# Kernel optimization log

Hardware: AMD Instinct MI355X
Metric: run time of the kernel (lower is better)

## Reference

```python
import jax, jax.numpy as jnp
import numpy as np

B, NVIS, NHID, NCLASS = 2048, 2048, 1024, 64


def setup_inputs() -> dict:
    key = jax.random.key(0)
    k1, k2, k3, k4, k5 = jax.random.split(key, 5)
    return {
        "v": jax.random.normal(k1, (B, NVIS), dtype=jnp.float32),
        "W": jax.random.normal(k2, (NVIS, NHID), dtype=jnp.float32),
        "c": jax.random.normal(k3, (1, NHID), dtype=jnp.float32),
        "d": jax.random.normal(k4, (1, NCLASS), dtype=jnp.float32),
        "U": jax.random.normal(k5, (NCLASS, NHID), dtype=jnp.float32),
    }


def reference(v, W, c, d, U):
    # precomputed_factor: [B, nhid]
    pre = jnp.matmul(v, W) + c
    # class free energies F[b, y] = d[0, y] + sum_j softplus(pre[b, j] + U[y, j])
    # broadcast to [B, nclass, nhid], reduce over hidden units
    F = d[0] + jnp.sum(jax.nn.softplus(pre[:, None, :] + U[None, :, :]), axis=-1)  # [B, nclass]
    # pairwise normalization 1 / sum_d exp(F_d - F_c) == softmax(F) along classes
    class_probs = jax.nn.softmax(F, axis=1)
    max_idx = jnp.argmax(class_probs, axis=1)
    one_hot = jax.nn.one_hot(max_idx, U.shape[0], dtype=jnp.int32)
    return class_probs, one_hot
```

## Files before the change

### kernel.cpp

```cpp
#include <hip/hip_runtime.h>

constexpr int kB    = 2048;
constexpr int kVIS  = 2048;
constexpr int kHID  = 1024;
constexpr int kCLS  = 64;
constexpr float kLog2e = 1.4426950408889634f;

typedef __attribute__((ext_vector_type(8))) short bf16x8;
typedef __attribute__((ext_vector_type(4))) float f32x4;

typedef __attribute__((address_space(3))) unsigned       as3_u32;
typedef __attribute__((address_space(1))) const unsigned as1_u32;

__device__ __forceinline__ void g2lds16(const void* g, void* l) {
    __builtin_amdgcn_global_load_lds((as1_u32*)g, (as3_u32*)l, 16, 0, 0);
}

__device__ __forceinline__ unsigned short f2bf(float x) {
    unsigned u = __float_as_uint(x);
    u += 0x7fffu + ((u >> 16) & 1u);
    return (unsigned short)(u >> 16);
}
__device__ __forceinline__ float bf2f(unsigned short h) {
    return __uint_as_float(((unsigned)h) << 16);
}

__global__ __launch_bounds__(256) void prep_all(const float* __restrict__ v,
                                                const float* __restrict__ W,
                                                const float* __restrict__ U,
                                                unsigned short* __restrict__ vh,
                                                unsigned short* __restrict__ vl,
                                                unsigned short* __restrict__ wth,
                                                unsigned short* __restrict__ wtl,
                                                float* __restrict__ Ut) {
    __shared__ float T[32][33];
    const int bx = blockIdx.x;
    if (bx < 4096) {
        const int i = (bx * 256 + threadIdx.x) * 4;
        const float4 xv = *(const float4*)(v + i);
        ushort4 h, l;
        h.x = f2bf(xv.x); l.x = f2bf(xv.x - bf2f(h.x));
        h.y = f2bf(xv.y); l.y = f2bf(xv.y - bf2f(h.y));
        h.z = f2bf(xv.z); l.z = f2bf(xv.z - bf2f(h.z));
        h.w = f2bf(xv.w); l.w = f2bf(xv.w - bf2f(h.w));
        *(ushort4*)(vh + i) = h;
        *(ushort4*)(vl + i) = l;
    } else if (bx < 6144) {
        const int b = bx - 4096;
        const int n0 = (b & 31) * 32, k0 = (b >> 5) * 32;
        const int c = threadIdx.x & 31, r0 = threadIdx.x >> 5;
#pragma unroll
        for (int p = 0; p < 4; ++p) {
            const int r = r0 + p * 8;
            T[r][c] = W[(size_t)(k0 + r) * kHID + n0 + c];
        }
        __syncthreads();
#pragma unroll
        for (int p = 0; p < 4; ++p) {
            const int rr = r0 + p * 8;
            const float x = T[c][rr];
            const unsigned short h = f2bf(x);
            const unsigned short l = f2bf(x - bf2f(h));
            const size_t o = (size_t)(n0 + rr) * kVIS + k0 + c;
            wth[o] = h;
            wtl[o] = l;
        }
    } else {
        const int id = (bx - 6144) * 256 + threadIdx.x;
        const int j = id >> 6, y = id & 63;
        Ut[id] = U[(size_t)y * kHID + j] * kLog2e;
    }
}

__global__ __launch_bounds__(256) void gemm_fused(const unsigned short* __restrict__ vh,
                                                  const unsigned short* __restrict__ vl,
                                                  const unsigned short* __restrict__ wth,
                                                  const unsigned short* __restrict__ wtl,
                                                  const float* __restrict__ cvec,
                                                  const float* __restrict__ Ut,
                                                  float* __restrict__ Fpart) {
    __shared__ __align__(16) union SMem {
        unsigned short stage[4][64 * 64];
        float ps[64][68];
    } smem;
    unsigned short* Ah = smem.stage[0];
    unsigned short* Al = smem.stage[1];
    unsigned short* Bh = smem.stage[2];
    unsigned short* Bl = smem.stage[3];

    const int tid = threadIdx.x;
    const int lane = tid & 63, wave = tid >> 6;
    const int m0 = blockIdx.y * 64, n0 = blockIdx.x * 64;
    const int wm = (wave >> 1) * 32, wn = (wave & 1) * 32;

    const int r0 = tid >> 3, r1 = r0 + 32;
    const int oc = (((tid & 7) ^ ((tid >> 3) & 7)) << 3);
    const size_t ga0 = (size_t)(m0 + r0) * kVIS + oc;
    const size_t ga1 = (size_t)(m0 + r1) * kVIS + oc;
    const size_t gb0 = (size_t)(n0 + r0) * kVIS + oc;
    const size_t gb1 = (size_t)(n0 + r1) * kVIS + oc;
    const int l0 = (r0 << 6) + ((tid & 7) << 3);
    const int l1 = (r1 << 6) + ((tid & 7) << 3);

    const int fm = lane & 15, fq = lane >> 4;
    const int rx = fm & 7;
    const int a0r = (wm + fm) << 6,  a1r = (wm + 16 + fm) << 6;
    const int b0r = (wn + fm) << 6,  b1r = (wn + 16 + fm) << 6;

    f32x4 acc[2][2] = {};

    for (int k0 = 0; k0 < kVIS; k0 += 64) {
        __syncthreads();
        g2lds16(vh + ga0 + k0, Ah + l0);
        g2lds16(vh + ga1 + k0, Ah + l1);
        g2lds16(vl + ga0 + k0, Al + l0);
        g2lds16(vl + ga1 + k0, Al + l1);
        g2lds16(wth + gb0 + k0, Bh + l0);
        g2lds16(wth + gb1 + k0, Bh + l1);
        g2lds16(wtl + gb0 + k0, Bl + l0);
        g2lds16(wtl + gb1 + k0, Bl + l1);
        __syncthreads();
#pragma unroll
        for (int kk = 0; kk < 64; kk += 32) {
            const int p = (((kk >> 3) + fq) ^ rx) << 3;
            const bf16x8 ah0 = *(const bf16x8*)(Ah + a0r + p);
            const bf16x8 ah1 = *(const bf16x8*)(Ah + a1r + p);
            const bf16x8 al0 = *(const bf16x8*)(Al + a0r + p);
            const bf16x8 al1 = *(const bf16x8*)(Al + a1r + p);
            const bf16x8 bh0 = *(const bf16x8*)(Bh + b0r + p);
            const bf16x8 bh1 = *(const bf16x8*)(Bh + b1r + p);
            const bf16x8 bl0 = *(const bf16x8*)(Bl + b0r + p);
            const bf16x8 bl1 = *(const bf16x8*)(Bl + b1r + p);
            acc[0][0] = __builtin_amdgcn_mfma_f32_16x16x32_bf16(ah0, bh0, acc[0][0], 0, 0, 0);
            acc[0][0] = __builtin_amdgcn_mfma_f32_16x16x32_bf16(ah0, bl0, acc[0][0], 0, 0, 0);
            acc[0][0] = __builtin_amdgcn_mfma_f32_16x16x32_bf16(al0, bh0, acc[0][0], 0, 0, 0);
            acc[0][1] = __builtin_amdgcn_mfma_f32_16x16x32_bf16(ah0, bh1, acc[0][1], 0, 0, 0);
            acc[0][1] = __builtin_amdgcn_mfma_f32_16x16x32_bf16(ah0, bl1, acc[0][1], 0, 0, 0);
            acc[0][1] = __builtin_amdgcn_mfma_f32_16x16x32_bf16(al0, bh1, acc[0][1], 0, 0, 0);
            acc[1][0] = __builtin_amdgcn_mfma_f32_16x16x32_bf16(ah1, bh0, acc[1][0], 0, 0, 0);
            acc[1][0] = __builtin_amdgcn_mfma_f32_16x16x32_bf16(ah1, bl0, acc[1][0], 0, 0, 0);
            acc[1][0] = __builtin_amdgcn_mfma_f32_16x16x32_bf16(al1, bh0, acc[1][0], 0, 0, 0);
            acc[1][1] = __builtin_amdgcn_mfma_f32_16x16x32_bf16(ah1, bh1, acc[1][1], 0, 0, 0);
            acc[1][1] = __builtin_amdgcn_mfma_f32_16x16x32_bf16(ah1, bl1, acc[1][1], 0, 0, 0);
            acc[1][1] = __builtin_amdgcn_mfma_f32_16x16x32_bf16(al1, bh1, acc[1][1], 0, 0, 0);
        }
    }

    __syncthreads();
#pragma unroll
    for (int j = 0; j < 2; ++j) {
        const int col = wn + j * 16 + fm;
        const float cv = cvec[n0 + col];
#pragma unroll
        for (int i = 0; i < 2; ++i) {
            const int rbase = wm + i * 16 + fq * 4;
#pragma unroll
            for (int r = 0; r < 4; ++r)
                smem.ps[rbase + r][col] = (acc[i][j][r] + cv) * kLog2e;
        }
    }
    __syncthreads();

    const float* UtN = Ut + (size_t)n0 * kCLS;
    float relu[16], prod[16];
#pragma unroll
    for (int rr = 0; rr < 16; ++rr) { relu[rr] = 0.f; prod[rr] = 1.f; }

    for (int jc = 0; jc < 64; jc += 8) {
        float u[8];
#pragma unroll
        for (int q = 0; q < 8; ++q) u[q] = UtN[(jc + q) * kCLS + lane];
#pragma unroll
        for (int rr = 0; rr < 16; ++rr) {
            const float4 p0 = *(const float4*)&smem.ps[wave * 16 + rr][jc];
            const float4 p1 = *(const float4*)&smem.ps[wave * 16 + rr][jc + 4];
            const float pv[8] = {p0.x, p0.y, p0.z, p0.w, p1.x, p1.y, p1.z, p1.w};
#pragma unroll
            for (int q = 0; q < 8; ++q) {
                const float t = pv[q] + u[q];
                const float e = __builtin_amdgcn_exp2f(-fabsf(t));
                prod[rr] = __builtin_fmaf(prod[rr], e, prod[rr]);
                relu[rr] += fmaxf(t, 0.f);
            }
        }
    }
#pragma unroll
    for (int rr = 0; rr < 16; ++rr) {
        const float contrib = relu[rr] + __builtin_amdgcn_logf(prod[rr]);
        Fpart[((size_t)blockIdx.x * kB + m0 + wave * 16 + rr) * kCLS + lane] = contrib;
    }
}

__global__ __launch_bounds__(256) void softmax_final(const float* __restrict__ Fpart,
                                                     const float* __restrict__ dvec,
                                                     float* __restrict__ out) {
    const int tid = threadIdx.x;
    const int lane = tid & 63, wave = tid >> 6;
    const int row = blockIdx.x * 4 + wave;
    double s = 0.0;
#pragma unroll
    for (int k = 0; k < kHID / 64; ++k)
        s += (double)Fpart[((size_t)k * kB + row) * kCLS + lane];
    const float G = (float)s + dvec[lane] * kLog2e;

    float m = G;
    int mi = lane;
#pragma unroll
    for (int off = 32; off; off >>= 1) {
        const float om = __shfl_xor(m, off);
        const int   oi = __shfl_xor(mi, off);
        if (om > m || (om == m && oi < mi)) { m = om; mi = oi; }
    }
    const float e2 = __builtin_amdgcn_exp2f(G - m);
    float ssum = e2;
#pragma unroll
    for (int off = 32; off; off >>= 1) ssum += __shfl_xor(ssum, off);
    out[(size_t)row * kCLS + lane] = e2 / ssum;
    out[(size_t)kB * kCLS + (size_t)row * kCLS + lane] = (lane == mi) ? 1.0f : 0.0f;
}

constexpr int BM = 64, BN = 64, BK = 16;

__global__ __launch_bounds__(256) void gemm_vw(const float* __restrict__ V,
                                               const float* __restrict__ Wm,
                                               const float* __restrict__ cvec,
                                               float* __restrict__ pre) {
    __shared__ float As[BK][BM + 4];
    __shared__ float Bs[BK][BN + 4];
    const int tid = threadIdx.x;
    const int tx = tid & 15, ty = tid >> 4;
    const int m0 = blockIdx.y * BM, n0 = blockIdx.x * BN;
    const int arow = tid >> 2, acol = (tid & 3) << 2;
    const int brow = tid >> 4, bcol = (tid & 15) << 2;
    const float* vptr = V + (size_t)(m0 + arow) * kVIS + acol;
    const float* wptr = Wm + (size_t)brow * kHID + n0 + bcol;
    float acc[4][4] = {};
    for (int k0 = 0; k0 < kVIS; k0 += BK) {
        const float4 a4 = *(const float4*)(vptr + k0);
        const float4 b4 = *(const float4*)(wptr + (size_t)k0 * kHID);
        __syncthreads();
        As[acol + 0][arow] = a4.x; As[acol + 1][arow] = a4.y;
        As[acol + 2][arow] = a4.z; As[acol + 3][arow] = a4.w;
        *(float4*)&Bs[brow][bcol] = b4;
        __syncthreads();
#pragma unroll
        for (int k = 0; k < BK; ++k) {
            const float4 av = *(const float4*)&As[k][ty << 2];
            const float4 bv = *(const float4*)&Bs[k][tx << 2];
            const float a[4] = {av.x, av.y, av.z, av.w};
            const float b[4] = {bv.x, bv.y, bv.z, bv.w};
#pragma unroll
            for (int i = 0; i < 4; ++i)
#pragma unroll
                for (int j = 0; j < 4; ++j) acc[i][j] += a[i] * b[j];
        }
    }
#pragma unroll
    for (int i = 0; i < 4; ++i) {
        const int row = m0 + (ty << 2) + i;
        const int col = n0 + (tx << 2);
        const float4 cv = *(const float4*)(cvec + col);
        float4 o;
        o.x = acc[i][0] + cv.x; o.y = acc[i][1] + cv.y;
        o.z = acc[i][2] + cv.z; o.w = acc[i][3] + cv.w;
        *(float4*)(pre + (size_t)row * kHID + col) = o;
    }
}

__device__ __forceinline__ float softplus_f(float x) {
    return fmaxf(x, 0.f) + __logf(1.f + __expf(-fabsf(x)));
}

__global__ __launch_bounds__(256) void classify(const float* __restrict__ pre,
                                                const float* __restrict__ U,
                                                const float* __restrict__ dvec,
                                                float* __restrict__ out) {
    __shared__ float preS[4][kHID];
    __shared__ float Fs[4][kCLS];
    const int tid = threadIdx.x;
    const int lane = tid & 63, wave = tid >> 6;
    const int b0 = blockIdx.x * 4;
    const float4* src = (const float4*)(pre + (size_t)b0 * kHID);
    float4* dst = (float4*)preS;
    for (int i = tid; i < kHID; i += 256) dst[i] = src[i];
    __syncthreads();
    for (int yi = 0; yi < 16; ++yi) {
        const int y = (wave << 4) + yi;
        const float* Uy = U + (size_t)y * kHID;
        float a0 = 0.f, a1 = 0.f, a2 = 0.f, a3 = 0.f;
#pragma unroll
        for (int it = 0; it < kHID / 64; ++it) {
            const int j = lane + (it << 6);
            const float u = Uy[j];
            a0 += softplus_f(preS[0][j] + u);
            a1 += softplus_f(preS[1][j] + u);
            a2 += softplus_f(preS[2][j] + u);
            a3 += softplus_f(preS[3][j] + u);
        }
        double d0 = a0, d1 = a1, d2 = a2, d3 = a3;
#pragma unroll
        for (int off = 32; off; off >>= 1) {
            d0 += __shfl_xor(d0, off); d1 += __shfl_xor(d1, off);
            d2 += __shfl_xor(d2, off); d3 += __shfl_xor(d3, off);
        }
        if (lane == 0) {
            const float dy = dvec[y];
            Fs[0][y] = (float)d0 + dy; Fs[1][y] = (float)d1 + dy;
            Fs[2][y] = (float)d2 + dy; Fs[3][y] = (float)d3 + dy;
        }
    }
    __syncthreads();
    const float F = Fs[wave][lane];
    float m = F; int mi = lane;
#pragma unroll
    for (int off = 32; off; off >>= 1) {
        const float om = __shfl_xor(m, off);
        const int oi = __shfl_xor(mi, off);
        if (om > m || (om == m && oi < mi)) { m = om; mi = oi; }
    }
    const float e = __expf(F - m);
    float s = e;
#pragma unroll
    for (int off = 32; off; off >>= 1) s += __shfl_xor(s, off);
    const int row = b0 + wave;
    out[(size_t)row * kCLS + lane] = e / s;
    out[(size_t)kB * kCLS + (size_t)row * kCLS + lane] = (lane == mi) ? 1.0f : 0.0f;
}

extern "C" void kernel_launch(void* const* d_in, const int* in_sizes, int n_in,
                              void* d_out, int out_size, void* d_ws, size_t ws_size,
                              hipStream_t stream) {
    const float* v = (const float*)d_in[0];
    const float* W = (const float*)d_in[1];
    const float* c = (const float*)d_in[2];
    const float* d = (const float*)d_in[3];
    const float* U = (const float*)d_in[4];
    float* out = (float*)d_out;
    char* ws = (char*)d_ws;

    const size_t need = 33816576;
    if (ws_size >= need) {
        unsigned short* vh  = (unsigned short*)(ws);
        unsigned short* vl  = (unsigned short*)(ws + 8388608);
        unsigned short* wth = (unsigned short*)(ws + 16777216);
        unsigned short* wtl = (unsigned short*)(ws + 20971520);
        float* Ut    = (float*)(ws + 25165824);
        float* Fpart = (float*)(ws + 25427968);
        prep_all<<<6400, 256, 0, stream>>>(v, W, U, vh, vl, wth, wtl, Ut);
        gemm_fused<<<dim3(kHID / 64, kB / 64), 256, 0, stream>>>(vh, vl, wth, wtl, c, Ut, Fpart);
        softmax_final<<<kB / 4, 256, 0, stream>>>(Fpart, d, out);
    } else {
        float* pre = (float*)ws;
        gemm_vw<<<dim3(kHID / BN, kB / BM), 256, 0, stream>>>(v, W, c, pre);
        classify<<<kB / 4, 256, 0, stream>>>(pre, U, d, out);
    }
}
```

Baseline: 136.0 us.

## Fuse softmax into GEMM via last-block counters, double K stage, packed epilogue

Doubles the per-iteration K stage to 128 by loading two 64-wide slices before each barrier, which halves the number of sync points at the cost of twice the LDS footprint. The U table is repacked so each lane reads float4 chunks, and the softplus epilogue is written with two-wide float vectors so the compiler can emit packed math. The separate softmax kernel is folded into the GEMM: per-row-block atomic counters, zeroed in the prep kernel, let the last-finishing block compute the softmax and argmax. This removes a kernel launch but serializes that tail work onto one block per row group, and it only runs when the workspace has room for the counters.

After: 172.5 us. 26.8% more time.

```diff
diff --git a/kernel.cpp b/kernel.cpp
--- a/kernel.cpp
+++ b/kernel.cpp
@@ -8,6 +8,7 @@
 
 typedef __attribute__((ext_vector_type(8))) short bf16x8;
 typedef __attribute__((ext_vector_type(4))) float f32x4;
+typedef __attribute__((ext_vector_type(2))) float f32x2;
 
 typedef __attribute__((address_space(3))) unsigned       as3_u32;
 typedef __attribute__((address_space(1))) const unsigned as1_u32;
@@ -32,7 +33,8 @@
                                                 unsigned short* __restrict__ vl,
                                                 unsigned short* __restrict__ wth,
                                                 unsigned short* __restrict__ wtl,
-                                                float* __restrict__ Ut) {
+                                                float* __restrict__ Utp,
+                                                int* __restrict__ ctrs) {
     __shared__ float T[32][33];
     const int bx = blockIdx.x;
     if (bx < 4096) {
@@ -65,10 +67,12 @@
             wth[o] = h;
             wtl[o] = l;
         }
-    } else {
+    } else if (bx < 6400) {
         const int id = (bx - 6144) * 256 + threadIdx.x;
         const int j = id >> 6, y = id & 63;
-        Ut[id] = U[(size_t)y * kHID + j] * kLog2e;
+        Utp[(((j >> 2) * kCLS + y) << 2) + (j & 3)] = U[(size_t)y * kHID + j] * kLog2e;
+    } else {
+        if (ctrs && threadIdx.x < 64) ctrs[threadIdx.x] = 0;
     }
 }
 
@@ -77,16 +81,16 @@
                                                   const unsigned short* __restrict__ wth,
                                                   const unsigned short* __restrict__ wtl,
                                                   const float* __restrict__ cvec,
-                                                  const float* __restrict__ Ut,
-                                                  float* __restrict__ Fpart) {
+                                                  const float* __restrict__ Utp,
+                                                  const float* __restrict__ dvec,
+                                                  float* __restrict__ Fpart,
+                                                  int* __restrict__ ctrs,
+                                                  float* __restrict__ out) {
     __shared__ __align__(16) union SMem {
-        unsigned short stage[4][64 * 64];
+        unsigned short stage[8][64 * 64];
         float ps[64][68];
     } smem;
-    unsigned short* Ah = smem.stage[0];
-    unsigned short* Al = smem.stage[1];
-    unsigned short* Bh = smem.stage[2];
-    unsigned short* Bl = smem.stage[3];
+    __shared__ int lastFlag;
 
     const int tid = threadIdx.x;
     const int lane = tid & 63, wave = tid >> 6;
@@ -109,40 +113,55 @@
 
     f32x4 acc[2][2] = {};
 
-    for (int k0 = 0; k0 < kVIS; k0 += 64) {
+    for (int k0 = 0; k0 < kVIS; k0 += 128) {
         __syncthreads();
-        g2lds16(vh + ga0 + k0, Ah + l0);
-        g2lds16(vh + ga1 + k0, Ah + l1);
-        g2lds16(vl + ga0 + k0, Al + l0);
-        g2lds16(vl + ga1 + k0, Al + l1);
-        g2lds16(wth + gb0 + k0, Bh + l0);
-        g2lds16(wth + gb1 + k0, Bh + l1);
-        g2lds16(wtl + gb0 + k0, Bl + l0);
-        g2lds16(wtl + gb1 + k0, Bl + l1);
+#pragma unroll
+        for (int h = 0; h < 2; ++h) {
+            const int ko = k0 + (h << 6);
+            unsigned short* Ah = smem.stage[h * 4 + 0];
+            unsigned short* Al = smem.stage[h * 4 + 1];
+            unsigned short* Bh = smem.stage[h * 4 + 2];
+            unsigned short* Bl = smem.stage[h * 4 + 3];
+            g2lds16(vh + ga0 + ko, Ah + l0);
+            g2lds16(vh + ga1 + ko, Ah + l1);
+            g2lds16(vl + ga0 + ko, Al + l0);
+            g2lds16(vl + ga1 + ko, Al + l1);
+            g2lds16(wth + gb0 + ko, Bh + l0);
+            g2lds16(wth + gb1 + ko, Bh + l1);
+            g2lds16(wtl + gb0 + ko, Bl + l0);
+            g2lds16(wtl + gb1 + ko, Bl + l1);
+        }
         __syncthreads();
 #pragma unroll
-        for (int kk = 0; kk < 64; kk += 32) {
-            const int p = (((kk >> 3) + fq) ^ rx) << 3;
-            const bf16x8 ah0 = *(const bf16x8*)(Ah + a0r + p);
-            const bf16x8 ah1 = *(const bf16x8*)(Ah + a1r + p);
-            const bf16x8 al0 = *(const bf16x8*)(Al + a0r + p);
-            const bf16x8 al1 = *(const bf16x8*)(Al + a1r + p);
-            const bf16x8 bh0 = *(const bf16x8*)(Bh + b0r + p);
-            const bf16x8 bh1 = *(const bf16x8*)(Bh + b1r + p);
-            const bf16x8 bl0 = *(const bf16x8*)(Bl + b0r + p);
-            const bf16x8 bl1 = *(const bf16x8*)(Bl + b1r + p);
-            acc[0][0] = __builtin_amdgcn_mfma_f32_16x16x32_bf16(ah0, bh0, acc[0][0], 0, 0, 0);
-            acc[0][0] = __builtin_amdgcn_mfma_f32_16x16x32_bf16(ah0, bl0, acc[0][0], 0, 0, 0);
-            acc[0][0] = __builtin_amdgcn_mfma_f32_16x16x32_bf16(al0, bh0, acc[0][0], 0, 0, 0);
-            acc[0][1] = __builtin_amdgcn_mfma_f32_16x16x32_bf16(ah0, bh1, acc[0][1], 0, 0, 0);
-            acc[0][1] = __builtin_amdgcn_mfma_f32_16x16x32_bf16(ah0, bl1, acc[0][1], 0, 0, 0);
-            acc[0][1] = __builtin_amdgcn_mfma_f32_16x16x32_bf16(al0, bh1, acc[0][1], 0, 0, 0);
-            acc[1][0] = __builtin_amdgcn_mfma_f32_16x16x32_bf16(ah1, bh0, acc[1][0], 0, 0, 0);
-            acc[1][0] = __builtin_amdgcn_mfma_f32_16x16x32_bf16(ah1, bl0, acc[1][0], 0, 0, 0);
-            acc[1][0] = __builtin_amdgcn_mfma_f32_16x16x32_bf16(al1, bh0, acc[1][0], 0, 0, 0);
-            acc[1][1] = __builtin_amdgcn_mfma_f32_16x16x32_bf16(ah1, bh1, acc[1][1], 0, 0, 0);
-            acc[1][1] = __builtin_amdgcn_mfma_f32_16x16x32_bf16(ah1, bl1, acc[1][1], 0, 0, 0);
-            acc[1][1] = __builtin_amdgcn_mfma_f32_16x16x32_bf16(al1, bh1, acc[1][1], 0, 0, 0);
+        for (int h = 0; h < 2; ++h) {
+            const unsigned short* Ah = smem.stage[h * 4 + 0];
+            const unsigned short* Al = smem.stage[h * 4 + 1];
+            const unsigned short* Bh = smem.stage[h * 4 + 2];
+            const unsigned short* Bl = smem.stage[h * 4 + 3];
+#pragma unroll
+            for (int kk = 0; kk < 64; kk += 32) {
+                const int p = (((kk >> 3) + fq) ^ rx) << 3;
+                const bf16x8 ah0 = *(const bf16x8*)(Ah + a0r + p);
+                const bf16x8 ah1 = *(const bf16x8*)(Ah + a1r + p);
+                const bf16x8 al0 = *(const bf16x8*)(Al + a0r + p);
+                const bf16x8 al1 = *(const bf16x8*)(Al + a1r + p);
+                const bf16x8 bh0 = *(const bf16x8*)(Bh + b0r + p);
+                const bf16x8 bh1 = *(const bf16x8*)(Bh + b1r + p);
+                const bf16x8 bl0 = *(const bf16x8*)(Bl + b0r + p);
+                const bf16x8 bl1 = *(const bf16x8*)(Bl + b1r + p);
+                acc[0][0] = __builtin_amdgcn_mfma_f32_16x16x32_bf16(ah0, bh0, acc[0][0], 0, 0, 0);
+                acc[0][0] = __builtin_amdgcn_mfma_f32_16x16x32_bf16(ah0, bl0, acc[0][0], 0, 0, 0);
+                acc[0][0] = __builtin_amdgcn_mfma_f32_16x16x32_bf16(al0, bh0, acc[0][0], 0, 0, 0);
+                acc[0][1] = __builtin_amdgcn_mfma_f32_16x16x32_bf16(ah0, bh1, acc[0][1], 0, 0, 0);
+                acc[0][1] = __builtin_amdgcn_mfma_f32_16x16x32_bf16(ah0, bl1, acc[0][1], 0, 0, 0);
+                acc[0][1] = __builtin_amdgcn_mfma_f32_16x16x32_bf16(al0, bh1, acc[0][1], 0, 0, 0);
+                acc[1][0] = __builtin_amdgcn_mfma_f32_16x16x32_bf16(ah1, bh0, acc[1][0], 0, 0, 0);
+                acc[1][0] = __builtin_amdgcn_mfma_f32_16x16x32_bf16(ah1, bl0, acc[1][0], 0, 0, 0);
+                acc[1][0] = __builtin_amdgcn_mfma_f32_16x16x32_bf16(al1, bh0, acc[1][0], 0, 0, 0);
+                acc[1][1] = __builtin_amdgcn_mfma_f32_16x16x32_bf16(ah1, bh1, acc[1][1], 0, 0, 0);
+                acc[1][1] = __builtin_amdgcn_mfma_f32_16x16x32_bf16(ah1, bl1, acc[1][1], 0, 0, 0);
+                acc[1][1] = __builtin_amdgcn_mfma_f32_16x16x32_bf16(al1, bh1, acc[1][1], 0, 0, 0);
+            }
         }
     }
 
@@ -161,33 +180,76 @@
     }
     __syncthreads();
 
-    const float* UtN = Ut + (size_t)n0 * kCLS;
-    float relu[16], prod[16];
-#pragma unroll
-    for (int rr = 0; rr < 16; ++rr) { relu[rr] = 0.f; prod[rr] = 1.f; }
-
+    const float4* Utp4 = (const float4*)(Utp + (size_t)n0 * kCLS * 4 / 4 * 4);
+    const int q0 = (n0 >> 2);
+    f32x2 relu2[16], prod2[16];
+#pragma unroll
+    for (int rr = 0; rr < 16; ++rr) { relu2[rr] = (f32x2)(0.f); prod2[rr] = (f32x2)(1.f); }
+
+    const f32x2 zero2 = (f32x2)(0.f);
     for (int jc = 0; jc < 64; jc += 8) {
-        float u[8];
-#pragma unroll
-        for (int q = 0; q < 8; ++q) u[q] = UtN[(jc + q) * kCLS + lane];
+        const float4 ua = ((const float4*)Utp)[(q0 + (jc >> 2) + 0) * kCLS + lane];
+        const float4 ub = ((const float4*)Utp)[(q0 + (jc >> 2) + 1) * kCLS + lane];
+        const f32x2 u01 = {ua.x, ua.y}, u23 = {ua.z, ua.w};
+        const f32x2 u45 = {ub.x, ub.y}, u67 = {ub.z, ub.w};
 #pragma unroll
         for (int rr = 0; rr < 16; ++rr) {
             const float4 p0 = *(const float4*)&smem.ps[wave * 16 + rr][jc];
             const float4 p1 = *(const float4*)&smem.ps[wave * 16 + rr][jc + 4];
-            const float pv[8] = {p0.x, p0.y, p0.z, p0.w, p1.x, p1.y, p1.z, p1.w};
-#pragma unroll
-            for (int q = 0; q < 8; ++q) {
-                const float t = pv[q] + u[q];
-                const float e = __builtin_amdgcn_exp2f(-fabsf(t));
-                prod[rr] = __builtin_fmaf(prod[rr], e, prod[rr]);
-                relu[rr] += fmaxf(t, 0.f);
+            f32x2 tp[4];
+            tp[0] = (f32x2){p0.x, p0.y} + u01;
+            tp[1] = (f32x2){p0.z, p0.w} + u23;
+            tp[2] = (f32x2){p1.x, p1.y} + u45;
+            tp[3] = (f32x2){p1.z, p1.w} + u67;
+#pragma unroll
+            for (int g = 0; g < 4; ++g) {
+                const f32x2 t = tp[g];
+                f32x2 e;
+                e.x = __builtin_amdgcn_exp2f(-__builtin_fabsf(t.x));
+                e.y = __builtin_amdgcn_exp2f(-__builtin_fabsf(t.y));
+                prod2[rr] = __builtin_elementwise_fma(prod2[rr], e, prod2[rr]);
+                relu2[rr] += __builtin_elementwise_max(t, zero2);
             }
         }
     }
 #pragma unroll
     for (int rr = 0; rr < 16; ++rr) {
-        const float contrib = relu[rr] + __builtin_amdgcn_logf(prod[rr]);
+        const float contrib = relu2[rr].x + relu2[rr].y +
+                              __builtin_amdgcn_logf(prod2[rr].x * prod2[rr].y);
         Fpart[((size_t)blockIdx.x * kB + m0 + wave * 16 + rr) * kCLS + lane] = contrib;
+    }
+
+    if (!ctrs) return;
+    __syncthreads();
+    if (tid == 0) {
+        __threadfence();
+        lastFlag = (atomicAdd(&ctrs[blockIdx.y], 1) == 15);
+    }
+    __syncthreads();
+    if (!lastFlag) return;
+    __threadfence();
+
+    for (int rr = 0; rr < 16; ++rr) {
+        const int row = m0 + wave * 16 + rr;
+        double s = 0.0;
+#pragma unroll
+        for (int kc = 0; kc < 16; ++kc)
+            s += (double)Fpart[((size_t)kc * kB + row) * kCLS + lane];
+        const float G = (float)s + dvec[lane] * kLog2e;
+        float m = G;
+        int mi = lane;
+#pragma unroll
+        for (int off = 32; off; off >>= 1) {
+            const float om = __shfl_xor(m, off);
+            const int   oi = __shfl_xor(mi, off);
+            if (om > m || (om == m && oi < mi)) { m = om; mi = oi; }
+        }
+        const float e2 = __builtin_amdgcn_exp2f(G - m);
+        float ssum = e2;
+#pragma unroll
+        for (int off = 32; off; off >>= 1) ssum += __shfl_xor(ssum, off);
+        out[(size_t)row * kCLS + lane] = e2 / ssum;
+        out[(size_t)kB * kCLS + (size_t)row * kCLS + lane] = (lane == mi) ? 1.0f : 0.0f;
     }
 }
 
@@ -202,7 +264,6 @@
     for (int k = 0; k < kHID / 64; ++k)
         s += (double)Fpart[((size_t)k * kB + row) * kCLS + lane];
     const float G = (float)s + dvec[lane] * kLog2e;
-
     float m = G;
     int mi = lane;
 #pragma unroll
@@ -338,17 +399,20 @@
     float* out = (float*)d_out;
     char* ws = (char*)d_ws;
 
-    const size_t need = 33816576;
+    const size_t need  = 33816576;
+    const size_t need2 = need + 256;
     if (ws_size >= need) {
         unsigned short* vh  = (unsigned short*)(ws);
         unsigned short* vl  = (unsigned short*)(ws + 8388608);
         unsigned short* wth = (unsigned short*)(ws + 16777216);
         unsigned short* wtl = (unsigned short*)(ws + 20971520);
-        float* Ut    = (float*)(ws + 25165824);
+        float* Utp   = (float*)(ws + 25165824);
         float* Fpart = (float*)(ws + 25427968);
-        prep_all<<<6400, 256, 0, stream>>>(v, W, U, vh, vl, wth, wtl, Ut);
-        gemm_fused<<<dim3(kHID / 64, kB / 64), 256, 0, stream>>>(vh, vl, wth, wtl, c, Ut, Fpart);
-        softmax_final<<<kB / 4, 256, 0, stream>>>(Fpart, d, out);
+        int* ctrs    = (ws_size >= need2) ? (int*)(ws + need) : nullptr;
+        prep_all<<<6401, 256, 0, stream>>>(v, W, U, vh, vl, wth, wtl, Utp, ctrs);
+        gemm_fused<<<dim3(kHID / 64, kB / 64), 256, 0, stream>>>(vh, vl, wth, wtl, c, Utp,
+                                                                 d, Fpart, ctrs, out);
+        if (!ctrs) softmax_final<<<kB / 4, 256, 0, stream>>>(Fpart, d, out);
     } else {
         float* pre = (float*)ws;
         gemm_vw<<<dim3(kHID / BN, kB / BM), 256, 0, stream>>>(v, W, c, pre);
```
